# Performance work log

Hardware: AMD Instinct MI355X
Metric: run time of the kernel (lower is better)

## Reference

```python
import jax, jax.numpy as jnp
import numpy as np

N, E, G = 40000, 400000, 40
DIN, DH, DOUT = 128, 256, 128
NEG_SLOPE = 0.2  # PyG GATConv default leaky_relu slope


def _gat_layer(h_in, src, dst, W, a_src, a_dst, b, num_nodes):
    # h_in: [N, din]; src/dst: [E'] (self loops included); W: [din, dout]
    h = h_in @ W                                   # [N, dout]
    al_s = h @ a_src                               # [N]
    al_d = h @ a_dst                               # [N]
    e = jax.nn.leaky_relu(al_s[src] + al_d[dst], NEG_SLOPE)  # [E']
    # scatter-softmax over incoming edges of each dst node (stable)
    m = jax.ops.segment_max(e, dst, num_segments=num_nodes)
    ex = jnp.exp(e - m[dst])
    denom = jax.ops.segment_sum(ex, dst, num_segments=num_nodes)
    alpha = ex / denom[dst]                        # [E']
    out = jax.ops.segment_sum(h[src] * alpha[:, None], dst, num_segments=num_nodes)
    return out + b


def setup_inputs() -> dict:
    key = jax.random.key(0)
    ks = jax.random.split(key, 16)
    x = jax.random.normal(ks[0], (N, DIN), dtype=jnp.float32)
    edge_index = jax.random.randint(ks[1], (2, E), 0, N, dtype=jnp.int64)

    def lin(k, din, dout):
        return jax.random.normal(k, (din, dout), dtype=jnp.float32) / np.sqrt(din)

    def vec(k, d):
        return jax.random.normal(k, (d,), dtype=jnp.float32) / np.sqrt(d)

    return dict(
        x=x, edge_index=edge_index, num_graphs=G,
        W1=lin(ks[2], DIN, DH), a_src1=vec(ks[3], DH), a_dst1=vec(ks[4], DH), b1=jnp.zeros((DH,), jnp.float32),
        W2=lin(ks[5], DH, DH), a_src2=vec(ks[6], DH), a_dst2=vec(ks[7], DH), b2=jnp.zeros((DH,), jnp.float32),
        W3=lin(ks[8], DH, DOUT), a_src3=vec(ks[9], DOUT), a_dst3=vec(ks[10], DOUT), b3=jnp.zeros((DOUT,), jnp.float32),
    )


def reference(x, edge_index, num_graphs, W1, a_src1, a_dst1, b1, W2, a_src2, a_dst2, b2, W3, a_src3, a_dst3, b3):
    num_nodes = x.shape[0]
    # PyG GATConv adds self-loops by default
    loop = jnp.arange(num_nodes, dtype=edge_index.dtype)
    src = jnp.concatenate([edge_index[0], loop])
    dst = jnp.concatenate([edge_index[1], loop])

    h = jax.nn.relu(_gat_layer(x, src, dst, W1, a_src1, a_dst1, b1, num_nodes))
    # dropout is identity in eval mode
    h = jax.nn.relu(_gat_layer(h, src, dst, W2, a_src2, a_dst2, b2, num_nodes))
    h = _gat_layer(h, src, dst, W3, a_src3, a_dst3, b3, num_nodes)
    return h.reshape(num_graphs, num_nodes // num_graphs, -1)
```

## Files before the change

### kernel.cpp

```cpp
#include <hip/hip_runtime.h>
#include <hip/hip_bf16.h>
#include <type_traits>

typedef __attribute__((ext_vector_type(8))) short short8;
typedef __attribute__((ext_vector_type(4))) float f32x4;
typedef __attribute__((ext_vector_type(8))) unsigned short u16x8;

static __device__ __forceinline__ unsigned short f2b(float f) {
    unsigned int v = __float_as_uint(f);
    unsigned int r = (v + 0x7FFFu + ((v >> 16) & 1u)) >> 16;
    return (unsigned short)r;
}
static __device__ __forceinline__ float b2f(unsigned short u) {
    return __uint_as_float(((unsigned int)u) << 16);
}

__global__ void k_hist(const int* __restrict__ dst, int* __restrict__ cnt, int E) {
    int e = blockIdx.x * 256 + threadIdx.x;
    if (e < E) atomicAdd(&cnt[dst[e]], 1);
}

__global__ void k_assign(const int* __restrict__ cnt, int* __restrict__ begptr,
                         int* __restrict__ colidx, int* __restrict__ fill,
                         int* __restrict__ cursor, int n) {
    int i = blockIdx.x * 256 + threadIdx.x;
    int lane = threadIdx.x & 63;
    int c = (i < n) ? cnt[i] + 1 : 0;
    int s = c;
#pragma unroll
    for (int off = 1; off < 64; off <<= 1) {
        int v = __shfl_up(s, off);
        if (lane >= off) s += v;
    }
    int wavesum = __shfl(s, 63);
    int base = 0;
    if (lane == 63) base = atomicAdd(cursor, wavesum);
    base = __shfl(base, 63);
    int beg = base + s - c;
    if (i < n) { begptr[i] = beg; colidx[beg] = i; fill[i] = beg + 1; }
}

__global__ void k_scatter(const int* __restrict__ src, const int* __restrict__ dst,
                          int* __restrict__ fill, int* __restrict__ colidx, int E) {
    int e = blockIdx.x * 256 + threadIdx.x;
    if (e < E) {
        int s = src[e], d = dst[e];
        int pos = atomicAdd(&fill[d], 1);
        colidx[pos] = s;
    }
}

__global__ void k_transpose3(const float* __restrict__ w1, unsigned short* __restrict__ t1,
                             const float* __restrict__ w2, unsigned short* __restrict__ t2,
                             const float* __restrict__ w3, unsigned short* __restrict__ t3,
                             int K1, int N1, int K2, int N2, int K3, int N3) {
    int i = blockIdx.x * 256 + threadIdx.x;
    int n1 = K1 * N1, n2 = K2 * N2, n3 = K3 * N3;
    if (i < n1) {
        int k = i / N1, n = i % N1;
        t1[n * K1 + k] = f2b(w1[i]);
    } else if (i < n1 + n2) {
        int j = i - n1, k = j / N2, n = j % N2;
        t2[n * K2 + k] = f2b(w2[j]);
    } else if (i < n1 + n2 + n3) {
        int j = i - n1 - n2, k = j / N3, n = j % N3;
        t3[n * K3 + k] = f2b(w3[j]);
    }
}

template<int NC, typename AT>
__global__ __launch_bounds__(256) void k_gemm(const AT* __restrict__ A,
                                              const unsigned short* __restrict__ Bt,
                                              unsigned short* __restrict__ H,
                                              const float* __restrict__ asrc,
                                              const float* __restrict__ adst,
                                              float* __restrict__ als,
                                              float* __restrict__ ald,
                                              int K) {
    __shared__ unsigned short As[64][40];
    __shared__ unsigned short Bs[NC][40];
    __shared__ float sps[64], spd[64];
    const int tid  = threadIdx.x;
    const int lane = tid & 63;
    const int wv   = tid >> 6;
    const int rowBase = blockIdx.x * 64;
    const int quad = lane >> 4;
    const int l16  = lane & 15;
    constexpr int CG = NC / 32;
    const int wrow = (wv & 1) * 32;
    const int wcol = (wv >> 1) * (NC / 2);
    f32x4 acc[2][CG] = {};

    if (tid < 64) { sps[tid] = 0.f; spd[tid] = 0.f; }

    const int ar = tid >> 2;
    const int ak = (tid & 3) * 8;

    for (int kk = 0; kk < K; kk += 32) {
        if constexpr (std::is_same_v<AT, float>) {
            const float* ap = A + (size_t)(rowBase + ar) * K + kk + ak;
            f32x4 a0 = *(const f32x4*)ap;
            f32x4 a1 = *(const f32x4*)(ap + 4);
            short8 s;
#pragma unroll
            for (int v = 0; v < 4; v++) { s[v] = (short)f2b(a0[v]); s[4 + v] = (short)f2b(a1[v]); }
            *(short8*)&As[ar][ak] = s;
        } else {
            *(short8*)&As[ar][ak] = *(const short8*)(A + (size_t)(rowBase + ar) * K + kk + ak);
        }
#pragma unroll
        for (int c = tid; c < NC * 4; c += 256) {
            int br = c >> 2, bk = (c & 3) * 8;
            *(short8*)&Bs[br][bk] = *(const short8*)(Bt + (size_t)br * K + kk + bk);
        }
        __syncthreads();
        short8 af0 = *(const short8*)&As[wrow + l16][quad * 8];
        short8 af1 = *(const short8*)&As[wrow + 16 + l16][quad * 8];
#pragma unroll
        for (int cg = 0; cg < CG; cg++) {
            short8 bf = *(const short8*)&Bs[wcol + cg * 16 + l16][quad * 8];
            acc[0][cg] = __builtin_amdgcn_mfma_f32_16x16x32_bf16(af0, bf, acc[0][cg], 0, 0, 0);
            acc[1][cg] = __builtin_amdgcn_mfma_f32_16x16x32_bf16(af1, bf, acc[1][cg], 0, 0, 0);
        }
        __syncthreads();
    }

    float avs[CG], avd[CG];
#pragma unroll
    for (int cg = 0; cg < CG; cg++) {
        int gcol = wcol + cg * 16 + l16;
        avs[cg] = asrc[gcol];
        avd[cg] = adst[gcol];
#pragma unroll
        for (int rg = 0; rg < 2; rg++)
#pragma unroll
            for (int r = 0; r < 4; r++) {
                int grow = rowBase + wrow + rg * 16 + quad * 4 + r;
                H[(size_t)grow * NC + gcol] = f2b(acc[rg][cg][r]);
            }
    }
#pragma unroll
    for (int rg = 0; rg < 2; rg++)
#pragma unroll
        for (int r = 0; r < 4; r++) {
            float ps = 0.f, pd = 0.f;
#pragma unroll
            for (int cg = 0; cg < CG; cg++) { ps += acc[rg][cg][r] * avs[cg]; pd += acc[rg][cg][r] * avd[cg]; }
#pragma unroll
            for (int off = 8; off; off >>= 1) { ps += __shfl_xor(ps, off); pd += __shfl_xor(pd, off); }
            if (l16 == 0) {
                int lrow = wrow + rg * 16 + quad * 4 + r;
                atomicAdd(&sps[lrow], ps);
                atomicAdd(&spd[lrow], pd);
            }
        }
    __syncthreads();
    if (tid < 64) { als[rowBase + tid] = sps[tid]; ald[rowBase + tid] = spd[tid]; }
}

template<int DOUT, bool RELU, typename OutT>
__global__ __launch_bounds__(256) void k_edge(const unsigned short* __restrict__ h,
                                              const float* __restrict__ als,
                                              const float* __restrict__ ald,
                                              const int* __restrict__ begptr,
                                              const int* __restrict__ cnt,
                                              const int* __restrict__ colidx,
                                              const float* __restrict__ bias,
                                              OutT* __restrict__ out, int N) {
    int node = blockIdx.x * 4 + (threadIdx.x >> 6);
    if (node >= N) return;
    int lane = threadIdx.x & 63;
    int beg = begptr[node];
    int deg = cnt[node] + 1;
    float aldi = ald[node];

    float ex_lane = 0.f;
    int   s_lane = 0;
    float dsum = 0.f;
    for (int j = lane; j < deg; j += 64) {
        int s = colidx[beg + j];
        float e = als[s] + aldi;
        e = e > 0.f ? e : 0.2f * e;
        float ex = __expf(e);
        if (j < 64) { ex_lane = ex; s_lane = s; }
        dsum += ex;
    }
#pragma unroll
    for (int off = 32; off; off >>= 1) dsum += __shfl_xor(dsum, off);
    float inv = 1.0f / dsum;
    float w_lane = ex_lane * inv;

    constexpr int QV  = DOUT / 16;
    constexpr int NC8 = QV / 8;
    const int l16g    = lane & 15;
    const int quarter = lane >> 4;
    const size_t dimOff = (size_t)l16g * QV;
    float acc[QV] = {};
    int lim = deg < 64 ? deg : 64;
    for (int t = 0; 4 * t < lim; t++) {
        int idx = 4 * t + quarter;
        float wj = __shfl(w_lane, idx);
        int   sj = __shfl(s_lane, idx);
        const unsigned short* hp = h + (size_t)sj * DOUT + dimOff;
        u16x8 c[NC8];
#pragma unroll
        for (int u = 0; u < NC8; u++) c[u] = *(const u16x8*)(hp + 8 * u);
#pragma unroll
        for (int u = 0; u < NC8; u++)
#pragma unroll
            for (int v = 0; v < 8; v++) acc[8 * u + v] += wj * b2f(c[u][v]);
    }
    for (int j = 64; j < deg; j++) {
        int sj = colidx[beg + j];
        float e = als[sj] + aldi;
        e = e > 0.f ? e : 0.2f * e;
        float wj = __expf(e) * inv;
        if (quarter == 0) {
            const unsigned short* hp = h + (size_t)sj * DOUT + dimOff;
#pragma unroll
            for (int u = 0; u < NC8; u++) {
                u16x8 c = *(const u16x8*)(hp + 8 * u);
#pragma unroll
                for (int v = 0; v < 8; v++) acc[8 * u + v] += wj * b2f(c[v]);
            }
        }
    }
#pragma unroll
    for (int v = 0; v < QV; v++) {
        acc[v] += __shfl_xor(acc[v], 16);
        acc[v] += __shfl_xor(acc[v], 32);
    }

    if (quarter == 0) {
        if constexpr (std::is_same_v<OutT, float>) {
            float* op = out + (size_t)node * DOUT + dimOff;
#pragma unroll
            for (int u = 0; u < QV / 4; u++) {
                f32x4 bv = *(const f32x4*)(bias + dimOff + 4 * u);
                f32x4 ov;
#pragma unroll
                for (int v = 0; v < 4; v++) {
                    float val = acc[4 * u + v] + bv[v];
                    if (RELU) val = fmaxf(val, 0.f);
                    ov[v] = val;
                }
                *(f32x4*)(op + 4 * u) = ov;
            }
        } else {
            unsigned short* op = out + (size_t)node * DOUT + dimOff;
#pragma unroll
            for (int u = 0; u < NC8; u++) {
                u16x8 ov;
#pragma unroll
                for (int v = 0; v < 8; v++) {
                    float val = acc[8 * u + v] + bias[dimOff + 8 * u + v];
                    if (RELU) val = fmaxf(val, 0.f);
                    ov[v] = f2b(val);
                }
                *(u16x8*)(op + 8 * u) = ov;
            }
        }
    }
}

extern "C" void kernel_launch(void* const* d_in, const int* in_sizes, int n_in,
                              void* d_out, int out_size, void* d_ws, size_t ws_size,
                              hipStream_t stream) {
    const int DIN = 128, DH = 256, DOUT = 128;
    const int N = in_sizes[0] / DIN;
    const int E = in_sizes[1] / 2;

    const float* x   = (const float*)d_in[0];
    const int*   ei  = (const int*)d_in[1];
    const float* W1  = (const float*)d_in[3];
    const float* as1 = (const float*)d_in[4];
    const float* ad1 = (const float*)d_in[5];
    const float* b1  = (const float*)d_in[6];
    const float* W2  = (const float*)d_in[7];
    const float* as2 = (const float*)d_in[8];
    const float* ad2 = (const float*)d_in[9];
    const float* b2  = (const float*)d_in[10];
    const float* W3  = (const float*)d_in[11];
    const float* as3 = (const float*)d_in[12];
    const float* ad3 = (const float*)d_in[13];
    const float* b3  = (const float*)d_in[14];
    float* outp = (float*)d_out;

    char* ws = (char*)d_ws;
    size_t off = 0;
    auto carve = [&](size_t bytes) { char* p = ws + off; off = (off + bytes + 255) & ~(size_t)255; return p; };
    unsigned short* hbuf = (unsigned short*)carve((size_t)N * DH * 2);
    unsigned short* gbuf = (unsigned short*)carve((size_t)N * DH * 2);
    float* als  = (float*)carve((size_t)N * 4);
    float* ald  = (float*)carve((size_t)N * 4);
    unsigned short* wt1 = (unsigned short*)carve((size_t)DIN * DH * 2);
    unsigned short* wt2 = (unsigned short*)carve((size_t)DH * DH * 2);
    unsigned short* wt3 = (unsigned short*)carve((size_t)DH * DOUT * 2);
    int* cnt    = (int*)carve((size_t)N * 4);
    int* cursor = (int*)carve(256);
    int* begptr = (int*)carve((size_t)N * 4);
    int* fill   = (int*)carve((size_t)N * 4);
    int* colidx = (int*)carve((size_t)(E + N) * 4);
    (void)ws_size; (void)n_in; (void)out_size;

    const int* e_src = ei;
    const int* e_dst = ei + E;

    hipMemsetAsync(cnt, 0, (size_t)((char*)cursor - (char*)cnt) + 4, stream);

    {
        int tot = DIN * DH + DH * DH + DH * DOUT;
        k_transpose3<<<(tot + 255) / 256, 256, 0, stream>>>(W1, wt1, W2, wt2, W3, wt3,
                                                            DIN, DH, DH, DH, DH, DOUT);
    }

    k_hist<<<(E + 255) / 256, 256, 0, stream>>>(e_dst, cnt, E);
    k_assign<<<(N + 255) / 256, 256, 0, stream>>>(cnt, begptr, colidx, fill, cursor, N);
    k_scatter<<<(E + 255) / 256, 256, 0, stream>>>(e_src, e_dst, fill, colidx, E);

    const int nblk4 = (N + 3) / 4;
    const int mblk  = N / 64;

    k_gemm<256, float><<<mblk, 256, 0, stream>>>(x, wt1, hbuf, as1, ad1, als, ald, DIN);
    k_edge<256, true, unsigned short><<<nblk4, 256, 0, stream>>>(hbuf, als, ald, begptr, cnt, colidx, b1, gbuf, N);

    k_gemm<256, unsigned short><<<mblk, 256, 0, stream>>>(gbuf, wt2, hbuf, as2, ad2, als, ald, DH);
    k_edge<256, true, unsigned short><<<nblk4, 256, 0, stream>>>(hbuf, als, ald, begptr, cnt, colidx, b2, gbuf, N);

    k_gemm<128, unsigned short><<<mblk, 256, 0, stream>>>(gbuf, wt3, hbuf, as3, ad3, als, ald, DH);
    k_edge<128, false, float><<<nblk4, 256, 0, stream>>>(hbuf, als, ald, begptr, cnt, colidx, b3, outp, N);
}
```

Baseline: 301.6 us.

## Merge preprocessing launches and widen GEMM K-tile to 64

Combines the weight transpose with the degree histogram in one launch, and runs the CSR scatter inside the first GEMM launch as extra blocks, which removes two kernel launches and their serialization gaps. The GEMM body also doubles its K step from 32 to 64 per shared-memory stage, halving the number of loop iterations and barrier pairs. The cost is more shared memory per block (padded rows of 72), which may lower occupancy. Heterogeneous blocks sharing one launch can also leave the scheduler with an uneven mix of work.

```diff
diff --git a/kernel.cpp b/kernel.cpp
--- a/kernel.cpp
+++ b/kernel.cpp
@@ -15,9 +15,28 @@
     return __uint_as_float(((unsigned int)u) << 16);
 }
 
-__global__ void k_hist(const int* __restrict__ dst, int* __restrict__ cnt, int E) {
-    int e = blockIdx.x * 256 + threadIdx.x;
-    if (e < E) atomicAdd(&cnt[dst[e]], 1);
+__global__ void k_pre(const float* __restrict__ w1, unsigned short* __restrict__ t1,
+                      const float* __restrict__ w2, unsigned short* __restrict__ t2,
+                      const float* __restrict__ w3, unsigned short* __restrict__ t3,
+                      int K1, int N1, int K2, int N2, int K3, int N3,
+                      const int* __restrict__ dst, int* __restrict__ cnt, int E, int tblk) {
+    if ((int)blockIdx.x < tblk) {
+        int i = blockIdx.x * 256 + threadIdx.x;
+        int n1 = K1 * N1, n2 = K2 * N2, n3 = K3 * N3;
+        if (i < n1) {
+            int k = i / N1, n = i % N1;
+            t1[n * K1 + k] = f2b(w1[i]);
+        } else if (i < n1 + n2) {
+            int j = i - n1, k = j / N2, n = j % N2;
+            t2[n * K2 + k] = f2b(w2[j]);
+        } else if (i < n1 + n2 + n3) {
+            int j = i - n1 - n2, k = j / N3, n = j % N3;
+            t3[n * K3 + k] = f2b(w3[j]);
+        }
+    } else {
+        int e = (blockIdx.x - tblk) * 256 + threadIdx.x;
+        if (e < E) atomicAdd(&cnt[dst[e]], 1);
+    }
 }
 
 __global__ void k_assign(const int* __restrict__ cnt, int* __restrict__ begptr,
@@ -40,32 +59,107 @@
     if (i < n) { begptr[i] = beg; colidx[beg] = i; fill[i] = beg + 1; }
 }
 
-__global__ void k_scatter(const int* __restrict__ src, const int* __restrict__ dst,
-                          int* __restrict__ fill, int* __restrict__ colidx, int E) {
-    int e = blockIdx.x * 256 + threadIdx.x;
-    if (e < E) {
-        int s = src[e], d = dst[e];
-        int pos = atomicAdd(&fill[d], 1);
-        colidx[pos] = s;
-    }
-}
-
-__global__ void k_transpose3(const float* __restrict__ w1, unsigned short* __restrict__ t1,
-                             const float* __restrict__ w2, unsigned short* __restrict__ t2,
-                             const float* __restrict__ w3, unsigned short* __restrict__ t3,
-                             int K1, int N1, int K2, int N2, int K3, int N3) {
-    int i = blockIdx.x * 256 + threadIdx.x;
-    int n1 = K1 * N1, n2 = K2 * N2, n3 = K3 * N3;
-    if (i < n1) {
-        int k = i / N1, n = i % N1;
-        t1[n * K1 + k] = f2b(w1[i]);
-    } else if (i < n1 + n2) {
-        int j = i - n1, k = j / N2, n = j % N2;
-        t2[n * K2 + k] = f2b(w2[j]);
-    } else if (i < n1 + n2 + n3) {
-        int j = i - n1 - n2, k = j / N3, n = j % N3;
-        t3[n * K3 + k] = f2b(w3[j]);
-    }
+template<int NC, typename AT>
+static __device__ __forceinline__ void gemm_body(const AT* __restrict__ A,
+                                                 const unsigned short* __restrict__ Bt,
+                                                 unsigned short* __restrict__ H,
+                                                 const float* __restrict__ asrc,
+                                                 const float* __restrict__ adst,
+                                                 float* __restrict__ als,
+                                                 float* __restrict__ ald,
+                                                 int K, int blk) {
+    __shared__ unsigned short As[64][72];
+    __shared__ unsigned short Bs[NC][72];
+    __shared__ float sps[64], spd[64];
+    const int tid  = threadIdx.x;
+    const int lane = tid & 63;
+    const int wv   = tid >> 6;
+    const int rowBase = blk * 64;
+    const int quad = lane >> 4;
+    const int l16  = lane & 15;
+    constexpr int CG = NC / 32;
+    const int wrow = (wv & 1) * 32;
+    const int wcol = (wv >> 1) * (NC / 2);
+    f32x4 acc[2][CG] = {};
+
+    if (tid < 64) { sps[tid] = 0.f; spd[tid] = 0.f; }
+
+    const int ar = tid >> 2;
+    const int ak = (tid & 3) * 16;
+
+    for (int kk = 0; kk < K; kk += 64) {
+        if constexpr (std::is_same_v<AT, float>) {
+            const float* ap = A + (size_t)(rowBase + ar) * K + kk + ak;
+            f32x4 a0 = *(const f32x4*)ap;
+            f32x4 a1 = *(const f32x4*)(ap + 4);
+            f32x4 a2 = *(const f32x4*)(ap + 8);
+            f32x4 a3 = *(const f32x4*)(ap + 12);
+            short8 s0, s1;
+#pragma unroll
+            for (int v = 0; v < 4; v++) {
+                s0[v] = (short)f2b(a0[v]); s0[4 + v] = (short)f2b(a1[v]);
+                s1[v] = (short)f2b(a2[v]); s1[4 + v] = (short)f2b(a3[v]);
+            }
+            *(short8*)&As[ar][ak] = s0;
+            *(short8*)&As[ar][ak + 8] = s1;
+        } else {
+            const unsigned short* ap = A + (size_t)(rowBase + ar) * K + kk + ak;
+            *(short8*)&As[ar][ak]     = *(const short8*)ap;
+            *(short8*)&As[ar][ak + 8] = *(const short8*)(ap + 8);
+        }
+#pragma unroll
+        for (int c = tid; c < NC * 4; c += 256) {
+            int br = c >> 2, bk = (c & 3) * 16;
+            const unsigned short* bp = Bt + (size_t)br * K + kk + bk;
+            *(short8*)&Bs[br][bk]     = *(const short8*)bp;
+            *(short8*)&Bs[br][bk + 8] = *(const short8*)(bp + 8);
+        }
+        __syncthreads();
+#pragma unroll
+        for (int s = 0; s < 2; s++) {
+            short8 af0 = *(const short8*)&As[wrow + l16][s * 32 + quad * 8];
+            short8 af1 = *(const short8*)&As[wrow + 16 + l16][s * 32 + quad * 8];
+#pragma unroll
+            for (int cg = 0; cg < CG; cg++) {
+                short8 bf = *(const short8*)&Bs[wcol + cg * 16 + l16][s * 32 + quad * 8];
+                acc[0][cg] = __builtin_amdgcn_mfma_f32_16x16x32_bf16(af0, bf, acc[0][cg], 0, 0, 0);
+                acc[1][cg] = __builtin_amdgcn_mfma_f32_16x16x32_bf16(af1, bf, acc[1][cg], 0, 0, 0);
+            }
+        }
+        __syncthreads();
+    }
+
+    float avs[CG], avd[CG];
+#pragma unroll
+    for (int cg = 0; cg < CG; cg++) {
+        int gcol = wcol + cg * 16 + l16;
+        avs[cg] = asrc[gcol];
+        avd[cg] = adst[gcol];
+#pragma unroll
+        for (int rg = 0; rg < 2; rg++)
+#pragma unroll
+            for (int r = 0; r < 4; r++) {
+                int grow = rowBase + wrow + rg * 16 + quad * 4 + r;
+                H[(size_t)grow * NC + gcol] = f2b(acc[rg][cg][r]);
+            }
+    }
+#pragma unroll
+    for (int rg = 0; rg < 2; rg++)
+#pragma unroll
+        for (int r = 0; r < 4; r++) {
+            float ps = 0.f, pd = 0.f;
+#pragma unroll
+            for (int cg = 0; cg < CG; cg++) { ps += acc[rg][cg][r] * avs[cg]; pd += acc[rg][cg][r] * avd[cg]; }
+#pragma unroll
+            for (int off = 8; off; off >>= 1) { ps += __shfl_xor(ps, off); pd += __shfl_xor(pd, off); }
+            if (l16 == 0) {
+                int lrow = wrow + rg * 16 + quad * 4 + r;
+                atomicAdd(&sps[lrow], ps);
+                atomicAdd(&spd[lrow], pd);
+            }
+        }
+    __syncthreads();
+    if (tid < 64) { als[rowBase + tid] = sps[tid]; ald[rowBase + tid] = spd[tid]; }
 }
 
 template<int NC, typename AT>
@@ -75,87 +169,32 @@
                                               const float* __restrict__ asrc,
                                               const float* __restrict__ adst,
                                               float* __restrict__ als,
-                                              float* __restrict__ ald,
-                                              int K) {
-    __shared__ unsigned short As[64][40];
-    __shared__ unsigned short Bs[NC][40];
-    __shared__ float sps[64], spd[64];
-    const int tid  = threadIdx.x;
-    const int lane = tid & 63;
-    const int wv   = tid >> 6;
-    const int rowBase = blockIdx.x * 64;
-    const int quad = lane >> 4;
-    const int l16  = lane & 15;
-    constexpr int CG = NC / 32;
-    const int wrow = (wv & 1) * 32;
-    const int wcol = (wv >> 1) * (NC / 2);
-    f32x4 acc[2][CG] = {};
-
-    if (tid < 64) { sps[tid] = 0.f; spd[tid] = 0.f; }
-
-    const int ar = tid >> 2;
-    const int ak = (tid & 3) * 8;
-
-    for (int kk = 0; kk < K; kk += 32) {
-        if constexpr (std::is_same_v<AT, float>) {
-            const float* ap = A + (size_t)(rowBase + ar) * K + kk + ak;
-            f32x4 a0 = *(const f32x4*)ap;
-            f32x4 a1 = *(const f32x4*)(ap + 4);
-            short8 s;
-#pragma unroll
-            for (int v = 0; v < 4; v++) { s[v] = (short)f2b(a0[v]); s[4 + v] = (short)f2b(a1[v]); }
-            *(short8*)&As[ar][ak] = s;
-        } else {
-            *(short8*)&As[ar][ak] = *(const short8*)(A + (size_t)(rowBase + ar) * K + kk + ak);
-        }
-#pragma unroll
-        for (int c = tid; c < NC * 4; c += 256) {
-            int br = c >> 2, bk = (c & 3) * 8;
-            *(short8*)&Bs[br][bk] = *(const short8*)(Bt + (size_t)br * K + kk + bk);
-        }
-        __syncthreads();
-        short8 af0 = *(const short8*)&As[wrow + l16][quad * 8];
-        short8 af1 = *(const short8*)&As[wrow + 16 + l16][quad * 8];
-#pragma unroll
-        for (int cg = 0; cg < CG; cg++) {
-            short8 bf = *(const short8*)&Bs[wcol + cg * 16 + l16][quad * 8];
-            acc[0][cg] = __builtin_amdgcn_mfma_f32_16x16x32_bf16(af0, bf, acc[0][cg], 0, 0, 0);
-            acc[1][cg] = __builtin_amdgcn_mfma_f32_16x16x32_bf16(af1, bf, acc[1][cg], 0, 0, 0);
-        }
-        __syncthreads();
-    }
-
-    float avs[CG], avd[CG];
-#pragma unroll
-    for (int cg = 0; cg < CG; cg++) {
-        int gcol = wcol + cg * 16 + l16;
-        avs[cg] = asrc[gcol];
-        avd[cg] = adst[gcol];
-#pragma unroll
-        for (int rg = 0; rg < 2; rg++)
-#pragma unroll
-            for (int r = 0; r < 4; r++) {
-                int grow = rowBase + wrow + rg * 16 + quad * 4 + r;
-                H[(size_t)grow * NC + gcol] = f2b(acc[rg][cg][r]);
-            }
-    }
-#pragma unroll
-    for (int rg = 0; rg < 2; rg++)
-#pragma unroll
-        for (int r = 0; r < 4; r++) {
-            float ps = 0.f, pd = 0.f;
-#pragma unroll
-            for (int cg = 0; cg < CG; cg++) { ps += acc[rg][cg][r] * avs[cg]; pd += acc[rg][cg][r] * avd[cg]; }
-#pragma unroll
-            for (int off = 8; off; off >>= 1) { ps += __shfl_xor(ps, off); pd += __shfl_xor(pd, off); }
-            if (l16 == 0) {
-                int lrow = wrow + rg * 16 + quad * 4 + r;
-                atomicAdd(&sps[lrow], ps);
-                atomicAdd(&spd[lrow], pd);
-            }
-        }
-    __syncthreads();
-    if (tid < 64) { als[rowBase + tid] = sps[tid]; ald[rowBase + tid] = spd[tid]; }
+                                              float* __restrict__ ald, int K) {
+    gemm_body<NC, AT>(A, Bt, H, asrc, adst, als, ald, K, blockIdx.x);
+}
+
+template<int NC, typename AT>
+__global__ __launch_bounds__(256) void k_gemm_scatter(const AT* __restrict__ A,
+                                                      const unsigned short* __restrict__ Bt,
+                                                      unsigned short* __restrict__ H,
+                                                      const float* __restrict__ asrc,
+                                                      const float* __restrict__ adst,
+                                                      float* __restrict__ als,
+                                                      float* __restrict__ ald, int K, int gblk,
+                                                      const int* __restrict__ src,
+                                                      const int* __restrict__ dst,
+                                                      int* __restrict__ fill,
+                                                      int* __restrict__ colidx, int E) {
+    if ((int)blockIdx.x < gblk) {
+        gemm_body<NC, AT>(A, Bt, H, asrc, adst, als, ald, K, blockIdx.x);
+    } else {
+        int e = (blockIdx.x - gblk) * 256 + threadIdx.x;
+        if (e < E) {
+            int s = src[e], d = dst[e];
+            int pos = atomicAdd(&fill[d], 1);
+            colidx[pos] = s;
+        }
+    }
 }
 
 template<int DOUT, bool RELU, typename OutT>
@@ -308,20 +347,20 @@
 
     hipMemsetAsync(cnt, 0, (size_t)((char*)cursor - (char*)cnt) + 4, stream);
 
-    {
-        int tot = DIN * DH + DH * DH + DH * DOUT;
-        k_transpose3<<<(tot + 255) / 256, 256, 0, stream>>>(W1, wt1, W2, wt2, W3, wt3,
-                                                            DIN, DH, DH, DH, DH, DOUT);
-    }
-
-    k_hist<<<(E + 255) / 256, 256, 0, stream>>>(e_dst, cnt, E);
-    k_assign<<<(N + 255) / 256, 256, 0, stream>>>(cnt, begptr, colidx, fill, cursor, N);
-    k_scatter<<<(E + 255) / 256, 256, 0, stream>>>(e_src, e_dst, fill, colidx, E);
-
+    const int tot   = DIN * DH + DH * DH + DH * DOUT;
+    const int tblk  = (tot + 255) / 256;
+    const int eblk  = (E + 255) / 256;
     const int nblk4 = (N + 3) / 4;
     const int mblk  = N / 64;
 
-    k_gemm<256, float><<<mblk, 256, 0, stream>>>(x, wt1, hbuf, as1, ad1, als, ald, DIN);
+    k_pre<<<tblk + eblk, 256, 0, stream>>>(W1, wt1, W2, wt2, W3, wt3,
+                                           DIN, DH, DH, DH, DH, DOUT,
+                                           e_dst, cnt, E, tblk);
+    k_assign<<<(N + 255) / 256, 256, 0, stream>>>(cnt, begptr, colidx, fill, cursor, N);
+
+    k_gemm_scatter<256, float><<<mblk + eblk, 256, 0, stream>>>(
+        x, wt1, hbuf, as1, ad1, als, ald, DIN, mblk,
+        e_src, e_dst, fill, colidx, E);
     k_edge<256, true, unsigned short><<<nblk4, 256, 0, stream>>>(hbuf, als, ald, begptr, cnt, colidx, b1, gbuf, N);
 
     k_gemm<256, unsigned short><<<mblk, 256, 0, stream>>>(gbuf, wt2, hbuf, as2, ad2, als, ald, DH);
```

After: 292.6 us. 1.03x faster.
